# Performance work log

Measured on AMD Instinct MI355X. Metric: run time of the kernel, lower is better.

The kernel has to match this reference:

```python
import jax, jax.numpy as jnp
import numpy as np

NR_HEADS = 8


def segment_softmax(scores, indices, num_segments):
    # numerically stable softmax within each segment
    seg_max = jax.ops.segment_max(scores, indices, num_segments=num_segments)
    e = jnp.exp(scores - seg_max[indices])
    denom = jax.ops.segment_sum(e, indices, num_segments=num_segments)
    return e / denom[indices]


def setup_inputs() -> dict:
    key = jax.random.key(0)
    ks = jax.random.split(key, 10)
    n_ast, d, n_cfg = 500000, 128, 32768
    H, combined = NR_HEADS, 128
    w_scale = 1.0 / np.sqrt(d)
    return {
        "ast_nodes_encodings": jax.random.normal(ks[0], (n_ast, d), jnp.float32),
        "Wq": jax.random.normal(ks[1], (H, d, d), jnp.float32) * w_scale,
        "bq": jnp.zeros((H, d), jnp.float32),
        "Wk": jax.random.normal(ks[2], (H, d, d), jnp.float32) * w_scale,
        "bk": jnp.zeros((H, d), jnp.float32),
        "Wo": jax.random.normal(ks[3], (H * d, combined), jnp.float32) * (1.0 / np.sqrt(H * d)),
        "bo": jnp.zeros((combined,), jnp.float32),
        "ast_key": jax.random.randint(ks[4], (n_ast,), 0, n_ast, jnp.int32),
        "ast_value": jax.random.randint(ks[5], (n_ast,), 0, n_cfg, jnp.int32),
        "pdg_key": jnp.arange(n_cfg, dtype=jnp.int32),
        "pdg_value": jax.random.randint(ks[6], (n_cfg,), 0, n_ast, jnp.int32),
        "nr_cfg_nodes": n_cfg,
    }


def reference(ast_nodes_encodings, Wq, bq, Wk, bk, Wo, bo,
              ast_key, ast_value, pdg_key, pdg_value, nr_cfg_nodes):
    N = int(nr_cfg_nodes)
    d = ast_nodes_encodings.shape[1]
    inv_sqrt_d = 1.0 / np.sqrt(d)

    # Build per-PDG-node attention queries: gather sub-AST root encodings, scatter into [N, d]
    root_encodings = ast_nodes_encodings[pdg_value]                   # [N_map, d]
    attn_queries = jnp.zeros((N, d), ast_nodes_encodings.dtype).at[pdg_key].set(root_encodings)

    # Gather scattered inputs (one row per AST node assigned to a PDG node)
    values = ast_nodes_encodings[ast_key]                              # [E, d]
    indices = ast_value                                                # [E]

    # Multi-head scatter attention (ScatterCombiner with combining_method='attn')
    head_outs = []
    for h in range(NR_HEADS):  # small fixed head count; avoids [E, H, d] intermediates
        q = attn_queries @ Wq[h] + bq[h]                               # [N, d]
        k = values @ Wk[h] + bk[h]                                     # [E, d]
        scores = jnp.sum(q[indices] * k, axis=-1) * inv_sqrt_d         # [E]
        probs = segment_softmax(scores, indices, N)                    # [E]
        head_outs.append(jax.ops.segment_sum(probs[:, None] * values, indices, num_segments=N))

    combined = jnp.concatenate(head_outs, axis=-1) @ Wo + bo           # [N, combined_dim]
    return combined
```

## Files before the change

kernel.cpp:

```cpp
#include <hip/hip_runtime.h>
#include <hip/hip_bf16.h>
#include <cstdint>

typedef __hip_bfloat16 bf16;
typedef unsigned int uint;
typedef unsigned short ushort;

#define DEVI __device__ __forceinline__

DEVI float blo(uint u){ return __uint_as_float(u << 16); }
DEVI float bhi(uint u){ return __uint_as_float(u & 0xffff0000u); }
DEVI ushort f2b(float x){ uint u = __float_as_uint(x); uint r = (u + 0x7fffu + ((u >> 16) & 1u)) >> 16; return (ushort)r; }
DEVI uint pack2(float a, float b){ return (uint)f2b(a) | ((uint)f2b(b) << 16); }
DEVI float b2f(ushort h){ return __uint_as_float((uint)h << 16); }

typedef short bf16x8 __attribute__((ext_vector_type(8)));
typedef float f32x4  __attribute__((ext_vector_type(4)));

DEVI float grp8_sum(float x){
  int y;
  y = __builtin_amdgcn_update_dpp(0, __float_as_int(x), 0xB1, 0xF, 0xF, true);
  x += __int_as_float(y);
  y = __builtin_amdgcn_update_dpp(0, __float_as_int(x), 0x4E, 0xF, 0xF, true);
  x += __int_as_float(y);
  y = __builtin_amdgcn_update_dpp(0, __float_as_int(x), 0x141, 0xF, 0xF, true);
  x += __int_as_float(y);
  return x;
}

__global__ __launch_bounds__(256) void build_M(const float* __restrict__ Wq, const float* __restrict__ Wk,
                                               float* __restrict__ Mb){
  __shared__ float WkL[128*33];
  __shared__ float WqL[16*33];
  const int t = threadIdx.x;
  const int h = blockIdx.x >> 3, pg = blockIdx.x & 7, p0 = pg*16;
  const float* wk = Wk + (size_t)h*16384;
  const float* wq = Wq + ((size_t)h*128 + p0)*128;
  const int m = t & 127, half = t >> 7;
  float acc[8] = {0,0,0,0,0,0,0,0};
  for (int jc = 0; jc < 4; ++jc){
    __syncthreads();
    #pragma unroll
    for (int i = 0; i < 4; ++i){
      int g = t + 256*i;
      int mm = g >> 3, j0 = (g & 7)*4;
      float4 v = *(const float4*)(wk + mm*128 + jc*32 + j0);
      float* d = &WkL[mm*33 + j0];
      d[0] = v.x; d[1] = v.y; d[2] = v.z; d[3] = v.w;
    }
    {
      int e = t*2;
      int pr = e >> 5, jj = e & 31;
      float2 v = *(const float2*)(wq + pr*128 + jc*32 + jj);
      WqL[pr*33 + jj] = v.x; WqL[pr*33 + jj + 1] = v.y;
    }
    __syncthreads();
    for (int j = 0; j < 32; ++j){
      float wkv = WkL[m*33 + j];
      #pragma unroll
      for (int r = 0; r < 8; ++r)
        acc[r] = fmaf(WqL[(half*8 + r)*33 + j], wkv, acc[r]);
    }
  }
  #pragma unroll
  for (int r = 0; r < 8; ++r)
    Mb[(size_t)(p0 + half*8 + r)*1024 + h*128 + m] = acc[r];
}

__global__ void build_bias(const float* __restrict__ Wq, const float* __restrict__ Wk,
                           const float* __restrict__ bq, const float* __restrict__ bk,
                           float* __restrict__ cvec, float* __restrict__ uvec, float* __restrict__ sv){
  int h = blockIdx.x, m = threadIdx.x;
  const float* wkr = Wk + ((size_t)h*128 + m)*128;
  const float* wqr = Wq + ((size_t)h*128 + m)*128;
  const float* bqr = bq + h*128;
  const float* bkr = bk + h*128;
  float c = 0.f, u = 0.f;
  for (int j = 0; j < 128; ++j){
    c = fmaf(wkr[j], bqr[j], c);
    u = fmaf(wqr[j], bkr[j], u);
  }
  cvec[h*128 + m] = c;
  uvec[h*128 + m] = u;
  if (m == 0){
    float s = 0.f;
    for (int j = 0; j < 128; ++j) s = fmaf(bqr[j], bkr[j], s);
    sv[h] = s;
  }
}

__global__ void scatter_aq(const int* __restrict__ pk, const int* __restrict__ pv,
                           const float* __restrict__ ast, float* __restrict__ aq,
                           ushort* __restrict__ aqh, ushort* __restrict__ aql, int n_map){
  int i = blockIdx.x;
  if (i >= n_map) return;
  int k = pk[i], src = pv[i];
  int lane = threadIdx.x;
  float2 v = *(const float2*)(ast + (size_t)src*128 + 2*lane);
  *(float2*)(aq + (size_t)k*128 + 2*lane) = v;
  ushort h0 = f2b(v.x), h1 = f2b(v.y);
  ushort l0 = f2b(v.x - b2f(h0)), l1 = f2b(v.y - b2f(h1));
  *(uint*)(aqh + (size_t)k*128 + 2*lane) = (uint)h0 | ((uint)h1 << 16);
  *(uint*)(aql + (size_t)k*128 + 2*lane) = (uint)l0 | ((uint)l1 << 16);
}

__global__ void frag_pack(const float* __restrict__ S, uint4* __restrict__ D, int C, int ctn){
  const int b = blockIdx.x;
  const int ks = b / ctn, ct = b - ks*ctn;
  const int l = threadIdx.x;
  const int kb = ks*32 + (l >> 4)*8;
  const int c  = ct*16 + (l & 15);
  ushort hi[8], lo[8];
  #pragma unroll
  for (int j = 0; j < 8; ++j){
    float wv = S[(size_t)(kb + j)*C + c];
    ushort hh = f2b(wv);
    hi[j] = hh;
    lo[j] = f2b(wv - b2f(hh));
  }
  uint4 H, L;
  H.x = (uint)hi[0] | ((uint)hi[1] << 16);
  H.y = (uint)hi[2] | ((uint)hi[3] << 16);
  H.z = (uint)hi[4] | ((uint)hi[5] << 16);
  H.w = (uint)hi[6] | ((uint)hi[7] << 16);
  L.x = (uint)lo[0] | ((uint)lo[1] << 16);
  L.y = (uint)lo[2] | ((uint)lo[3] << 16);
  L.z = (uint)lo[4] | ((uint)lo[5] << 16);
  L.w = (uint)lo[6] | ((uint)lo[7] << 16);
  D[((size_t)b*2 + 0)*64 + l] = H;
  D[((size_t)b*2 + 1)*64 + l] = L;
}

__global__ __launch_bounds__(256, 1) void qt_mfma(const ushort* __restrict__ aqh, const ushort* __restrict__ aql,
                                                  const uint4* __restrict__ Mp, const float* __restrict__ cvec,
                                                  bf16* __restrict__ qt, int N){
  const int l = threadIdx.x & 63, w = threadIdx.x >> 6;
  const int lr = l & 15, lk = l >> 4;
  const int r0 = blockIdx.x*16;
  int ra = r0 + lr; if (ra > N-1) ra = N-1;
  const ushort* ph = aqh + (size_t)ra*128 + lk*8;
  const ushort* pl = aql + (size_t)ra*128 + lk*8;
  bf16x8 Ah[4], Al[4];
  #pragma unroll
  for (int ks = 0; ks < 4; ++ks){
    Ah[ks] = *(const bf16x8*)(ph + ks*32);
    Al[ks] = *(const bf16x8*)(pl + ks*32);
  }
  const int ct0 = w*16;
  for (int ct = 0; ct < 16; ++ct){
    const int ctg = ct0 + ct;
    f32x4 acc = {0.f, 0.f, 0.f, 0.f};
    #pragma unroll
    for (int ks = 0; ks < 4; ++ks){
      const uint4* q = Mp + ((size_t)(ks*64 + ctg)*2)*64 + l;
      bf16x8 Bh = *(const bf16x8*)q;
      bf16x8 Bl = *(const bf16x8*)(q + 64);
      acc = __builtin_amdgcn_mfma_f32_16x16x32_bf16(Ah[ks], Bh, acc, 0, 0, 0);
      acc = __builtin_amdgcn_mfma_f32_16x16x32_bf16(Al[ks], Bh, acc, 0, 0, 0);
      acc = __builtin_amdgcn_mfma_f32_16x16x32_bf16(Ah[ks], Bl, acc, 0, 0, 0);
    }
    const int cc = ctg*16 + lr;
    const float bv = cvec[cc];
    #pragma unroll
    for (int i = 0; i < 4; ++i){
      int rr = r0 + lk*4 + i;
      if (rr < N) ((ushort*)qt)[(size_t)rr*1024 + cc] = f2b(acc[i] + bv);
    }
  }
}

__global__ void qb_kernel(const float* __restrict__ aq, const float* __restrict__ uvec,
                          const float* __restrict__ sv, float* __restrict__ qb){
  int n = blockIdx.x, lane = threadIdx.x;
  int h = lane >> 3, g = lane & 7;
  const float* ar = aq + (size_t)n*128 + g*16;
  const float* ur = uvec + h*128 + g*16;
  float dot = 0.f;
  #pragma unroll
  for (int k = 0; k < 16; ++k) dot = fmaf(ar[k], ur[k], dot);
  dot += __shfl_xor(dot, 1);
  dot += __shfl_xor(dot, 2);
  dot += __shfl_xor(dot, 4);
  if (g == 0) qb[(size_t)n*8 + h] = dot + sv[h];
}

__global__ void count_edges(const int* __restrict__ av, int* __restrict__ counts, int E){
  int e = blockIdx.x*256 + threadIdx.x;
  if (e < E) atomicAdd(&counts[av[e]], 1);
}

__global__ void scan_offsets(const int* __restrict__ counts, int* __restrict__ offsets, int N){
  __shared__ int pa[1024];
  __shared__ int pb[1024];
  int t = threadIdx.x;
  int CH = (N + 1023) >> 10;
  int b = t*CH, e = b + CH;
  if (b > N) b = N;
  if (e > N) e = N;
  int s = 0;
  for (int i = b; i < e; ++i) s += counts[i];
  pa[t] = s;
  __syncthreads();
  int* src = pa; int* dst = pb;
  for (int off = 1; off < 1024; off <<= 1){
    int v = src[t];
    if (t >= off) v += src[t - off];
    __syncthreads();
    dst[t] = v;
    __syncthreads();
    int* tmp = src; src = dst; dst = tmp;
  }
  int run = src[t] - s;
  for (int i = b; i < e; ++i){ offsets[i] = run; run += counts[i]; }
  if (t == 1023) offsets[N] = src[1023];
}

__global__ void fill_edges(const int* __restrict__ av, const int* __restrict__ akey,
                           const int* __restrict__ offsets, int* __restrict__ cursor,
                           int* __restrict__ ridx, int E){
  int e = blockIdx.x*256 + threadIdx.x;
  if (e < E){
    int seg = av[e];
    int pos = offsets[seg] + atomicAdd(&cursor[seg], 1);
    ridx[pos] = akey[e];
  }
}

__global__ __launch_bounds__(256) void seg_attn(
    const bf16* __restrict__ qt, const float* __restrict__ qb,
    const int* __restrict__ offsets, const int* __restrict__ ridx,
    const float* __restrict__ ast, bf16* __restrict__ ho, int N)
{
  const int wid  = threadIdx.x >> 6;
  const int lane = threadIdx.x & 63;
  const int n = blockIdx.x*4 + wid;
  if (n >= N) return;
  const int beg = __builtin_amdgcn_readfirstlane(offsets[n]);
  const int end = __builtin_amdgcn_readfirstlane(offsets[n+1]);
  const int deg = end - beg;
  const int h = lane >> 3, g = lane & 7;

  const uint4* qp = (const uint4*)(qt + (size_t)n*1024 + h*128 + g*16);
  const uint4 qa = qp[0], qc = qp[1];
  const float4 q0 = make_float4(blo(qa.x), bhi(qa.x), blo(qa.y), bhi(qa.y));
  const float4 q1 = make_float4(blo(qa.z), bhi(qa.z), blo(qa.w), bhi(qa.w));
  const float4 q2 = make_float4(blo(qc.x), bhi(qc.x), blo(qc.y), bhi(qc.y));
  const float4 q3 = make_float4(blo(qc.z), bhi(qc.z), blo(qc.w), bhi(qc.w));
  const float qbv = qb[(size_t)n*8 + h];
  const float isd = 0.08838834764831845f;

  const int* rp = ridx + beg;

  float den = 0.f;
  float4 x0 = make_float4(0,0,0,0), x1 = x0, x2 = x0, x3 = x0;

  if (deg > 0){
    #define ROWP(ee) ((const float4*)(ast + (size_t)rp[(ee) < deg ? (ee) : deg-1]*128) + g*4)
    float4 A0, A1, A2, A3, B0, B1, B2, B3;
    { const float4* p = ROWP(0); A0 = p[0]; A1 = p[1]; A2 = p[2]; A3 = p[3]; }
    { const float4* p = ROWP(1); B0 = p[0]; B1 = p[1]; B2 = p[2]; B3 = p[3]; }
    int e = 0;
    for (; e + 1 < deg; e += 2){
      const float4 a0 = A0, a1 = A1, a2 = A2, a3 = A3;
      const float4 b0 = B0, b1 = B1, b2 = B2, b3 = B3;
      { const float4* p = ROWP(e + 2); A0 = p[0]; A1 = p[1]; A2 = p[2]; A3 = p[3]; }
      { const float4* p = ROWP(e + 3); B0 = p[0]; B1 = p[1]; B2 = p[2]; B3 = p[3]; }

      float dA = 0.f, dB = 0.f;
      dA = fmaf(a0.x, q0.x, dA); dA = fmaf(a0.y, q0.y, dA);
      dA = fmaf(a0.z, q0.z, dA); dA = fmaf(a0.w, q0.w, dA);
      dA = fmaf(a1.x, q1.x, dA); dA = fmaf(a1.y, q1.y, dA);
      dA = fmaf(a1.z, q1.z, dA); dA = fmaf(a1.w, q1.w, dA);
      dA = fmaf(a2.x, q2.x, dA); dA = fmaf(a2.y, q2.y, dA);
      dA = fmaf(a2.z, q2.z, dA); dA = fmaf(a2.w, q2.w, dA);
      dA = fmaf(a3.x, q3.x, dA); dA = fmaf(a3.y, q3.y, dA);
      dA = fmaf(a3.z, q3.z, dA); dA = fmaf(a3.w, q3.w, dA);
      dB = fmaf(b0.x, q0.x, dB); dB = fmaf(b0.y, q0.y, dB);
      dB = fmaf(b0.z, q0.z, dB); dB = fmaf(b0.w, q0.w, dB);
      dB = fmaf(b1.x, q1.x, dB); dB = fmaf(b1.y, q1.y, dB);
      dB = fmaf(b1.z, q1.z, dB); dB = fmaf(b1.w, q1.w, dB);
      dB = fmaf(b2.x, q2.x, dB); dB = fmaf(b2.y, q2.y, dB);
      dB = fmaf(b2.z, q2.z, dB); dB = fmaf(b2.w, q2.w, dB);
      dB = fmaf(b3.x, q3.x, dB); dB = fmaf(b3.y, q3.y, dB);
      dB = fmaf(b3.z, q3.z, dB); dB = fmaf(b3.w, q3.w, dB);
      dA = grp8_sum(dA);
      dB = grp8_sum(dB);

      const float pA = __expf((dA + qbv) * isd);
      const float pB = __expf((dB + qbv) * isd);
      den += pA; den += pB;

      x0.x = fmaf(pA, a0.x, x0.x); x0.y = fmaf(pA, a0.y, x0.y);
      x0.z = fmaf(pA, a0.z, x0.z); x0.w = fmaf(pA, a0.w, x0.w);
      x1.x = fmaf(pA, a1.x, x1.x); x1.y = fmaf(pA, a1.y, x1.y);
      x1.z = fmaf(pA, a1.z, x1.z); x1.w = fmaf(pA, a1.w, x1.w);
      x2.x = fmaf(pA, a2.x, x2.x); x2.y = fmaf(pA, a2.y, x2.y);
      x2.z = fmaf(pA, a2.z, x2.z); x2.w = fmaf(pA, a2.w, x2.w);
      x3.x = fmaf(pA, a3.x, x3.x); x3.y = fmaf(pA, a3.y, x3.y);
      x3.z = fmaf(pA, a3.z, x3.z); x3.w = fmaf(pA, a3.w, x3.w);
      x0.x = fmaf(pB, b0.x, x0.x); x0.y = fmaf(pB, b0.y, x0.y);
      x0.z = fmaf(pB, b0.z, x0.z); x0.w = fmaf(pB, b0.w, x0.w);
      x1.x = fmaf(pB, b1.x, x1.x); x1.y = fmaf(pB, b1.y, x1.y);
      x1.z = fmaf(pB, b1.z, x1.z); x1.w = fmaf(pB, b1.w, x1.w);
      x2.x = fmaf(pB, b2.x, x2.x); x2.y = fmaf(pB, b2.y, x2.y);
      x2.z = fmaf(pB, b2.z, x2.z); x2.w = fmaf(pB, b2.w, x2.w);
      x3.x = fmaf(pB, b3.x, x3.x); x3.y = fmaf(pB, b3.y, x3.y);
      x3.z = fmaf(pB, b3.z, x3.z); x3.w = fmaf(pB, b3.w, x3.w);
    }
    if (e < deg){
      const float4 a0 = A0, a1 = A1, a2 = A2, a3 = A3;
      float dA = 0.f;
      dA = fmaf(a0.x, q0.x, dA); dA = fmaf(a0.y, q0.y, dA);
      dA = fmaf(a0.z, q0.z, dA); dA = fmaf(a0.w, q0.w, dA);
      dA = fmaf(a1.x, q1.x, dA); dA = fmaf(a1.y, q1.y, dA);
      dA = fmaf(a1.z, q1.z, dA); dA = fmaf(a1.w, q1.w, dA);
      dA = fmaf(a2.x, q2.x, dA); dA = fmaf(a2.y, q2.y, dA);
      dA = fmaf(a2.z, q2.z, dA); dA = fmaf(a2.w, q2.w, dA);
      dA = fmaf(a3.x, q3.x, dA); dA = fmaf(a3.y, q3.y, dA);
      dA = fmaf(a3.z, q3.z, dA); dA = fmaf(a3.w, q3.w, dA);
      dA = grp8_sum(dA);
      const float pA = __expf((dA + qbv) * isd);
      den += pA;
      x0.x = fmaf(pA, a0.x, x0.x); x0.y = fmaf(pA, a0.y, x0.y);
      x0.z = fmaf(pA, a0.z, x0.z); x0.w = fmaf(pA, a0.w, x0.w);
      x1.x = fmaf(pA, a1.x, x1.x); x1.y = fmaf(pA, a1.y, x1.y);
      x1.z = fmaf(pA, a1.z, x1.z); x1.w = fmaf(pA, a1.w, x1.w);
      x2.x = fmaf(pA, a2.x, x2.x); x2.y = fmaf(pA, a2.y, x2.y);
      x2.z = fmaf(pA, a2.z, x2.z); x2.w = fmaf(pA, a2.w, x2.w);
      x3.x = fmaf(pA, a3.x, x3.x); x3.y = fmaf(pA, a3.y, x3.y);
      x3.z = fmaf(pA, a3.z, x3.z); x3.w = fmaf(pA, a3.w, x3.w);
    }
    #undef ROWP
  }
  const float r = (deg > 0) ? (1.f / den) : 0.f;

  uint4 o0, o1;
  o0.x = pack2(x0.x*r, x0.y*r); o0.y = pack2(x0.z*r, x0.w*r);
  o0.z = pack2(x1.x*r, x1.y*r); o0.w = pack2(x1.z*r, x1.w*r);
  o1.x = pack2(x2.x*r, x2.y*r); o1.y = pack2(x2.z*r, x2.w*r);
  o1.z = pack2(x3.x*r, x3.y*r); o1.w = pack2(x3.z*r, x3.w*r);
  uint4* hb = (uint4*)(ho + (size_t)n*1024 + h*128 + g*16);
  hb[0] = o0;
  hb[1] = o1;
}

__global__ __launch_bounds__(256, 1) void out_mfma(const bf16* __restrict__ ho, const uint4* __restrict__ Wp,
                                                   const float* __restrict__ bo, float* __restrict__ out, int N){
  const int l = threadIdx.x & 63, w = threadIdx.x >> 6;
  const int lr = l & 15, lk = l >> 4;
  const int r0 = blockIdx.x*128 + w*32;
  int ra = r0 + lr;      if (ra > N-1) ra = N-1;
  int rb = r0 + 16 + lr; if (rb > N-1) rb = N-1;
  const bf16* pa = ho + (size_t)ra*1024 + lk*8;
  const bf16* pb = ho + (size_t)rb*1024 + lk*8;
  const uint4* pw = Wp + l;

  f32x4 acc[2][8];
  #pragma unroll
  for (int i = 0; i < 2; ++i)
    #pragma unroll
    for (int c = 0; c < 8; ++c)
      #pragma unroll
      for (int j = 0; j < 4; ++j) acc[i][c][j] = 0.f;

  bf16x8 Aa[2], Ab[2], Ba[16], Bb[16];

  auto LD = [&](int ks, bf16x8* A, bf16x8* B){
    A[0] = *(const bf16x8*)(pa + ks*32);
    A[1] = *(const bf16x8*)(pb + ks*32);
    const uint4* q = pw + (size_t)ks*1024;
    #pragma unroll
    for (int u = 0; u < 16; ++u) B[u] = *(const bf16x8*)(q + (size_t)u*64);
  };
  auto MM = [&](bf16x8* A, bf16x8* B){
    #pragma unroll
    for (int c = 0; c < 8; ++c){
      acc[0][c] = __builtin_amdgcn_mfma_f32_16x16x32_bf16(A[0], B[2*c],   acc[0][c], 0, 0, 0);
      acc[1][c] = __builtin_amdgcn_mfma_f32_16x16x32_bf16(A[1], B[2*c],   acc[1][c], 0, 0, 0);
      acc[0][c] = __builtin_amdgcn_mfma_f32_16x16x32_bf16(A[0], B[2*c+1], acc[0][c], 0, 0, 0);
      acc[1][c] = __builtin_amdgcn_mfma_f32_16x16x32_bf16(A[1], B[2*c+1], acc[1][c], 0, 0, 0);
    }
  };

  LD(0, Aa, Ba);
  for (int ks = 0; ks < 32; ks += 2){
    LD(ks + 1, Ab, Bb);
    MM(Aa, Ba);
    if (ks + 2 < 32) LD(ks + 2, Aa, Ba);
    MM(Ab, Bb);
  }

  #pragma unroll
  for (int c = 0; c < 8; ++c){
    float bv = bo[c*16 + lr];
    #pragma unroll
    for (int rt = 0; rt < 2; ++rt){
      #pragma unroll
      for (int i = 0; i < 4; ++i){
        int rr = r0 + rt*16 + lk*4 + i;
        if (rr < N) out[(size_t)rr*128 + c*16 + lr] = acc[rt][c][i] + bv;
      }
    }
  }
}

extern "C" void kernel_launch(void* const* d_in, const int* in_sizes, int n_in,
                              void* d_out, int out_size, void* d_ws, size_t ws_size,
                              hipStream_t stream) {
  const float* ast = (const float*)d_in[0];
  const float* Wq  = (const float*)d_in[1];
  const float* bq  = (const float*)d_in[2];
  const float* Wk  = (const float*)d_in[3];
  const float* bk  = (const float*)d_in[4];
  const float* Wo  = (const float*)d_in[5];
  const float* bo  = (const float*)d_in[6];
  const int* ast_key   = (const int*)d_in[7];
  const int* ast_value = (const int*)d_in[8];
  const int* pdg_key   = (const int*)d_in[9];
  const int* pdg_value = (const int*)d_in[10];
  const int E     = in_sizes[7];
  const int n_map = in_sizes[9];
  const int N     = out_size / 128;
  float* out = (float*)d_out;

  char* w = (char*)d_ws;
  auto carve = [&](size_t bytes)->char*{
    char* p = w; w += (bytes + 255) & ~size_t(255); return p;
  };
  bf16*  qt      = (bf16*) carve((size_t)N*1024*2);
  float* aq      = (float*)carve((size_t)N*128*4);
  float* Mb      = (float*)carve((size_t)128*1024*4);
  float* cvec    = (float*)carve(1024*4);
  float* uvec    = (float*)carve(1024*4);
  float* sv      = (float*)carve(8*4);
  float* qb      = (float*)carve((size_t)N*8*4);
  int*   counts  = (int*)  carve((size_t)N*4);
  int*   offsets = (int*)  carve((size_t)(N+1)*4);
  int*   cursor  = (int*)  carve((size_t)N*4);
  int*   ridx    = (int*)  carve((size_t)E*4);
  bf16*  ho      = (bf16*) carve((size_t)N*1024*2);
  uint4* Wp      = (uint4*)carve((size_t)256*2*64*16);
  ushort* aqh    = (ushort*)carve((size_t)N*128*2);
  ushort* aql    = (ushort*)carve((size_t)N*128*2);
  uint4* Mp      = (uint4*)carve((size_t)256*2*64*16);
  (void)ws_size; (void)n_in;

  hipMemsetAsync(aq,     0, (size_t)N*128*4, stream);
  hipMemsetAsync(aqh,    0, (size_t)N*128*2, stream);
  hipMemsetAsync(aql,    0, (size_t)N*128*2, stream);
  hipMemsetAsync(counts, 0, (size_t)N*4, stream);
  hipMemsetAsync(cursor, 0, (size_t)N*4, stream);

  build_M   <<<64, 256, 0, stream>>>(Wq, Wk, Mb);
  build_bias<<<8, 128, 0, stream>>>(Wq, Wk, bq, bk, cvec, uvec, sv);
  frag_pack <<<256, 64, 0, stream>>>(Wo, Wp, 128, 8);
  scatter_aq<<<n_map, 64, 0, stream>>>(pdg_key, pdg_value, ast, aq, aqh, aql, n_map);
  frag_pack <<<256, 64, 0, stream>>>(Mb, Mp, 1024, 64);
  qt_mfma   <<<(N + 15)/16, 256, 0, stream>>>(aqh, aql, Mp, cvec, qt, N);
  qb_kernel <<<N, 64, 0, stream>>>(aq, uvec, sv, qb);
  count_edges<<<(E + 255)/256, 256, 0, stream>>>(ast_value, counts, E);
  scan_offsets<<<1, 1024, 0, stream>>>(counts, offsets, N);
  fill_edges<<<(E + 255)/256, 256, 0, stream>>>(ast_value, ast_key, offsets, cursor, ridx, E);
  seg_attn  <<<(N + 3)/4, 256, 0, stream>>>(qt, qb, offsets, ridx, ast, ho, N);
  out_mfma  <<<(N + 127)/128, 256, 0, stream>>>(ho, Wp, bo, out, N);
}
```

Measured before the change: 770.8 us.

## Retile qt_mfma for B reuse and remap seg_attn lanes to two heads

qt_mfma now gives each wave 32 rows and all 64 column tiles, double-buffering the packed M fragments so each B load feeds two row tiles instead of one. seg_attn maps 16 lanes per pair of heads, so each lane reads 8 floats of an AST row once and uses them for two heads. The per-head dot product is reduced across 16 lanes with row-shift DPP, exp is folded into exp2 with a prescaled constant, and up to six rows are prefetched ahead. The aim is less redundant global traffic for the M fragments and the gathered AST rows, and more loads in flight, at the cost of higher register pressure.

```diff
diff --git a/kernel.cpp b/kernel.cpp
--- a/kernel.cpp
+++ b/kernel.cpp
@@ -17,14 +17,12 @@
 typedef short bf16x8 __attribute__((ext_vector_type(8)));
 typedef float f32x4  __attribute__((ext_vector_type(4)));
 
-DEVI float grp8_sum(float x){
+DEVI float row16_sum(float x){
   int y;
-  y = __builtin_amdgcn_update_dpp(0, __float_as_int(x), 0xB1, 0xF, 0xF, true);
-  x += __int_as_float(y);
-  y = __builtin_amdgcn_update_dpp(0, __float_as_int(x), 0x4E, 0xF, 0xF, true);
-  x += __int_as_float(y);
-  y = __builtin_amdgcn_update_dpp(0, __float_as_int(x), 0x141, 0xF, 0xF, true);
-  x += __int_as_float(y);
+  y = __builtin_amdgcn_update_dpp(0, __float_as_int(x), 0x121, 0xF, 0xF, true); x += __int_as_float(y);
+  y = __builtin_amdgcn_update_dpp(0, __float_as_int(x), 0x122, 0xF, 0xF, true); x += __int_as_float(y);
+  y = __builtin_amdgcn_update_dpp(0, __float_as_int(x), 0x124, 0xF, 0xF, true); x += __int_as_float(y);
+  y = __builtin_amdgcn_update_dpp(0, __float_as_int(x), 0x128, 0xF, 0xF, true); x += __int_as_float(y);
   return x;
 }
 
@@ -136,36 +134,57 @@
                                                   bf16* __restrict__ qt, int N){
   const int l = threadIdx.x & 63, w = threadIdx.x >> 6;
   const int lr = l & 15, lk = l >> 4;
-  const int r0 = blockIdx.x*16;
-  int ra = r0 + lr; if (ra > N-1) ra = N-1;
-  const ushort* ph = aqh + (size_t)ra*128 + lk*8;
-  const ushort* pl = aql + (size_t)ra*128 + lk*8;
-  bf16x8 Ah[4], Al[4];
+  const int r0 = blockIdx.x*128 + w*32;
+  int ra = r0 + lr;      if (ra > N-1) ra = N-1;
+  int rb = r0 + 16 + lr; if (rb > N-1) rb = N-1;
+
+  bf16x8 Ah0[4], Al0[4], Ah1[4], Al1[4];
   #pragma unroll
   for (int ks = 0; ks < 4; ++ks){
-    Ah[ks] = *(const bf16x8*)(ph + ks*32);
-    Al[ks] = *(const bf16x8*)(pl + ks*32);
-  }
-  const int ct0 = w*16;
-  for (int ct = 0; ct < 16; ++ct){
-    const int ctg = ct0 + ct;
-    f32x4 acc = {0.f, 0.f, 0.f, 0.f};
+    Ah0[ks] = *(const bf16x8*)(aqh + (size_t)ra*128 + lk*8 + ks*32);
+    Al0[ks] = *(const bf16x8*)(aql + (size_t)ra*128 + lk*8 + ks*32);
+    Ah1[ks] = *(const bf16x8*)(aqh + (size_t)rb*128 + lk*8 + ks*32);
+    Al1[ks] = *(const bf16x8*)(aql + (size_t)rb*128 + lk*8 + ks*32);
+  }
+  const uint4* pw = Mp + l;
+
+  bf16x8 Ba[8], Bb[8];
+  auto LDB = [&](int ct, bf16x8* B){
     #pragma unroll
     for (int ks = 0; ks < 4; ++ks){
-      const uint4* q = Mp + ((size_t)(ks*64 + ctg)*2)*64 + l;
-      bf16x8 Bh = *(const bf16x8*)q;
-      bf16x8 Bl = *(const bf16x8*)(q + 64);
-      acc = __builtin_amdgcn_mfma_f32_16x16x32_bf16(Ah[ks], Bh, acc, 0, 0, 0);
-      acc = __builtin_amdgcn_mfma_f32_16x16x32_bf16(Al[ks], Bh, acc, 0, 0, 0);
-      acc = __builtin_amdgcn_mfma_f32_16x16x32_bf16(Ah[ks], Bl, acc, 0, 0, 0);
-    }
-    const int cc = ctg*16 + lr;
+      const uint4* q = pw + ((size_t)(ks*64 + ct)*2)*64;
+      B[ks*2]   = *(const bf16x8*)q;
+      B[ks*2+1] = *(const bf16x8*)(q + 64);
+    }
+  };
+  auto DO = [&](int ct, bf16x8* B){
+    f32x4 a0 = {0.f,0.f,0.f,0.f}, a1 = {0.f,0.f,0.f,0.f};
+    #pragma unroll
+    for (int ks = 0; ks < 4; ++ks){
+      a0 = __builtin_amdgcn_mfma_f32_16x16x32_bf16(Ah0[ks], B[2*ks],   a0, 0, 0, 0);
+      a1 = __builtin_amdgcn_mfma_f32_16x16x32_bf16(Ah1[ks], B[2*ks],   a1, 0, 0, 0);
+      a0 = __builtin_amdgcn_mfma_f32_16x16x32_bf16(Al0[ks], B[2*ks],   a0, 0, 0, 0);
+      a1 = __builtin_amdgcn_mfma_f32_16x16x32_bf16(Al1[ks], B[2*ks],   a1, 0, 0, 0);
+      a0 = __builtin_amdgcn_mfma_f32_16x16x32_bf16(Ah0[ks], B[2*ks+1], a0, 0, 0, 0);
+      a1 = __builtin_amdgcn_mfma_f32_16x16x32_bf16(Ah1[ks], B[2*ks+1], a1, 0, 0, 0);
+    }
+    const int cc = ct*16 + lr;
     const float bv = cvec[cc];
     #pragma unroll
     for (int i = 0; i < 4; ++i){
-      int rr = r0 + lk*4 + i;
-      if (rr < N) ((ushort*)qt)[(size_t)rr*1024 + cc] = f2b(acc[i] + bv);
-    }
+      int rr0 = r0 + lk*4 + i;
+      if (rr0 < N) ((ushort*)qt)[(size_t)rr0*1024 + cc] = f2b(a0[i] + bv);
+      int rr1 = r0 + 16 + lk*4 + i;
+      if (rr1 < N) ((ushort*)qt)[(size_t)rr1*1024 + cc] = f2b(a1[i] + bv);
+    }
+  };
+
+  LDB(0, Ba);
+  for (int ct = 0; ct < 64; ct += 2){
+    LDB(ct + 1, Bb);
+    DO(ct, Ba);
+    if (ct + 2 < 64) LDB(ct + 2, Ba);
+    DO(ct + 1, Bb);
   }
 }
 
@@ -238,110 +257,86 @@
   const int beg = __builtin_amdgcn_readfirstlane(offsets[n]);
   const int end = __builtin_amdgcn_readfirstlane(offsets[n+1]);
   const int deg = end - beg;
-  const int h = lane >> 3, g = lane & 7;
-
-  const uint4* qp = (const uint4*)(qt + (size_t)n*1024 + h*128 + g*16);
-  const uint4 qa = qp[0], qc = qp[1];
-  const float4 q0 = make_float4(blo(qa.x), bhi(qa.x), blo(qa.y), bhi(qa.y));
-  const float4 q1 = make_float4(blo(qa.z), bhi(qa.z), blo(qa.w), bhi(qa.w));
-  const float4 q2 = make_float4(blo(qc.x), bhi(qc.x), blo(qc.y), bhi(qc.y));
-  const float4 q3 = make_float4(blo(qc.z), bhi(qc.z), blo(qc.w), bhi(qc.w));
-  const float qbv = qb[(size_t)n*8 + h];
-  const float isd = 0.08838834764831845f;
+  const int grp = lane >> 4, d4 = lane & 15;
+  const int h0 = 2*grp, h1 = 2*grp + 1;
+
+  const ushort* qtp = (const ushort*)qt + (size_t)n*1024 + d4*8;
+  const uint4 Qa = *(const uint4*)(qtp + h0*128);
+  const uint4 Qb = *(const uint4*)(qtp + h1*128);
+  const float4 q0lo = make_float4(blo(Qa.x), bhi(Qa.x), blo(Qa.y), bhi(Qa.y));
+  const float4 q0hi = make_float4(blo(Qa.z), bhi(Qa.z), blo(Qa.w), bhi(Qa.w));
+  const float4 q1lo = make_float4(blo(Qb.x), bhi(Qb.x), blo(Qb.y), bhi(Qb.y));
+  const float4 q1hi = make_float4(blo(Qb.z), bhi(Qb.z), blo(Qb.w), bhi(Qb.w));
+  const float SC = 0.12751744886681336f;
+  const float qs0 = qb[(size_t)n*8 + h0] * SC;
+  const float qs1 = qb[(size_t)n*8 + h1] * SC;
 
   const int* rp = ridx + beg;
 
-  float den = 0.f;
-  float4 x0 = make_float4(0,0,0,0), x1 = x0, x2 = x0, x3 = x0;
+  float den0 = 0.f, den1 = 0.f;
+  float4 x0lo = make_float4(0,0,0,0), x0hi = x0lo, x1lo = x0lo, x1hi = x0lo;
 
   if (deg > 0){
-    #define ROWP(ee) ((const float4*)(ast + (size_t)rp[(ee) < deg ? (ee) : deg-1]*128) + g*4)
-    float4 A0, A1, A2, A3, B0, B1, B2, B3;
-    { const float4* p = ROWP(0); A0 = p[0]; A1 = p[1]; A2 = p[2]; A3 = p[3]; }
-    { const float4* p = ROWP(1); B0 = p[0]; B1 = p[1]; B2 = p[2]; B3 = p[3]; }
+#define LOADP(Pa0, Pa1, Pb0, Pb1, base) do { \
+    int iA = (base) < deg ? (base) : deg-1; \
+    int iB = (base)+1 < deg ? (base)+1 : deg-1; \
+    const float4* pA = (const float4*)(ast + (size_t)rp[iA]*128 + d4*8); \
+    const float4* pB = (const float4*)(ast + (size_t)rp[iB]*128 + d4*8); \
+    Pa0 = pA[0]; Pa1 = pA[1]; Pb0 = pB[0]; Pb1 = pB[1]; } while(0)
+
+#define C1(A0, A1) do { \
+    float s0, s1; \
+    s0 = A0.x*q0lo.x; s0 = fmaf(A0.y, q0lo.y, s0); s0 = fmaf(A0.z, q0lo.z, s0); s0 = fmaf(A0.w, q0lo.w, s0); \
+    s0 = fmaf(A1.x, q0hi.x, s0); s0 = fmaf(A1.y, q0hi.y, s0); s0 = fmaf(A1.z, q0hi.z, s0); s0 = fmaf(A1.w, q0hi.w, s0); \
+    s1 = A0.x*q1lo.x; s1 = fmaf(A0.y, q1lo.y, s1); s1 = fmaf(A0.z, q1lo.z, s1); s1 = fmaf(A0.w, q1lo.w, s1); \
+    s1 = fmaf(A1.x, q1hi.x, s1); s1 = fmaf(A1.y, q1hi.y, s1); s1 = fmaf(A1.z, q1hi.z, s1); s1 = fmaf(A1.w, q1hi.w, s1); \
+    s0 = row16_sum(s0); s1 = row16_sum(s1); \
+    const float p0 = exp2f(fmaf(s0, SC, qs0)); \
+    const float p1 = exp2f(fmaf(s1, SC, qs1)); \
+    den0 += p0; den1 += p1; \
+    x0lo.x = fmaf(p0, A0.x, x0lo.x); x0lo.y = fmaf(p0, A0.y, x0lo.y); \
+    x0lo.z = fmaf(p0, A0.z, x0lo.z); x0lo.w = fmaf(p0, A0.w, x0lo.w); \
+    x0hi.x = fmaf(p0, A1.x, x0hi.x); x0hi.y = fmaf(p0, A1.y, x0hi.y); \
+    x0hi.z = fmaf(p0, A1.z, x0hi.z); x0hi.w = fmaf(p0, A1.w, x0hi.w); \
+    x1lo.x = fmaf(p1, A0.x, x1lo.x); x1lo.y = fmaf(p1, A0.y, x1lo.y); \
+    x1lo.z = fmaf(p1, A0.z, x1lo.z); x1lo.w = fmaf(p1, A0.w, x1lo.w); \
+    x1hi.x = fmaf(p1, A1.x, x1hi.x); x1hi.y = fmaf(p1, A1.y, x1hi.y); \
+    x1hi.z = fmaf(p1, A1.z, x1hi.z); x1hi.w = fmaf(p1, A1.w, x1hi.w); \
+  } while(0)
+
+    float4 P0a0, P0a1, P0b0, P0b1;
+    float4 P1a0, P1a1, P1b0, P1b1;
+    float4 P2a0, P2a1, P2b0, P2b1;
+    LOADP(P0a0, P0a1, P0b0, P0b1, 0);
+    LOADP(P1a0, P1a1, P1b0, P1b1, 2);
+    LOADP(P2a0, P2a1, P2b0, P2b1, 4);
     int e = 0;
-    for (; e + 1 < deg; e += 2){
-      const float4 a0 = A0, a1 = A1, a2 = A2, a3 = A3;
-      const float4 b0 = B0, b1 = B1, b2 = B2, b3 = B3;
-      { const float4* p = ROWP(e + 2); A0 = p[0]; A1 = p[1]; A2 = p[2]; A3 = p[3]; }
-      { const float4* p = ROWP(e + 3); B0 = p[0]; B1 = p[1]; B2 = p[2]; B3 = p[3]; }
-
-      float dA = 0.f, dB = 0.f;
-      dA = fmaf(a0.x, q0.x, dA); dA = fmaf(a0.y, q0.y, dA);
-      dA = fmaf(a0.z, q0.z, dA); dA = fmaf(a0.w, q0.w, dA);
-      dA = fmaf(a1.x, q1.x, dA); dA = fmaf(a1.y, q1.y, dA);
-      dA = fmaf(a1.z, q1.z, dA); dA = fmaf(a1.w, q1.w, dA);
-      dA = fmaf(a2.x, q2.x, dA); dA = fmaf(a2.y, q2.y, dA);
-      dA = fmaf(a2.z, q2.z, dA); dA = fmaf(a2.w, q2.w, dA);
-      dA = fmaf(a3.x, q3.x, dA); dA = fmaf(a3.y, q3.y, dA);
-      dA = fmaf(a3.z, q3.z, dA); dA = fmaf(a3.w, q3.w, dA);
-      dB = fmaf(b0.x, q0.x, dB); dB = fmaf(b0.y, q0.y, dB);
-      dB = fmaf(b0.z, q0.z, dB); dB = fmaf(b0.w, q0.w, dB);
-      dB = fmaf(b1.x, q1.x, dB); dB = fmaf(b1.y, q1.y, dB);
-      dB = fmaf(b1.z, q1.z, dB); dB = fmaf(b1.w, q1.w, dB);
-      dB = fmaf(b2.x, q2.x, dB); dB = fmaf(b2.y, q2.y, dB);
-      dB = fmaf(b2.z, q2.z, dB); dB = fmaf(b2.w, q2.w, dB);
-      dB = fmaf(b3.x, q3.x, dB); dB = fmaf(b3.y, q3.y, dB);
-      dB = fmaf(b3.z, q3.z, dB); dB = fmaf(b3.w, q3.w, dB);
-      dA = grp8_sum(dA);
-      dB = grp8_sum(dB);
-
-      const float pA = __expf((dA + qbv) * isd);
-      const float pB = __expf((dB + qbv) * isd);
-      den += pA; den += pB;
-
-      x0.x = fmaf(pA, a0.x, x0.x); x0.y = fmaf(pA, a0.y, x0.y);
-      x0.z = fmaf(pA, a0.z, x0.z); x0.w = fmaf(pA, a0.w, x0.w);
-      x1.x = fmaf(pA, a1.x, x1.x); x1.y = fmaf(pA, a1.y, x1.y);
-      x1.z = fmaf(pA, a1.z, x1.z); x1.w = fmaf(pA, a1.w, x1.w);
-      x2.x = fmaf(pA, a2.x, x2.x); x2.y = fmaf(pA, a2.y, x2.y);
-      x2.z = fmaf(pA, a2.z, x2.z); x2.w = fmaf(pA, a2.w, x2.w);
-      x3.x = fmaf(pA, a3.x, x3.x); x3.y = fmaf(pA, a3.y, x3.y);
-      x3.z = fmaf(pA, a3.z, x3.z); x3.w = fmaf(pA, a3.w, x3.w);
-      x0.x = fmaf(pB, b0.x, x0.x); x0.y = fmaf(pB, b0.y, x0.y);
-      x0.z = fmaf(pB, b0.z, x0.z); x0.w = fmaf(pB, b0.w, x0.w);
-      x1.x = fmaf(pB, b1.x, x1.x); x1.y = fmaf(pB, b1.y, x1.y);
-      x1.z = fmaf(pB, b1.z, x1.z); x1.w = fmaf(pB, b1.w, x1.w);
-      x2.x = fmaf(pB, b2.x, x2.x); x2.y = fmaf(pB, b2.y, x2.y);
-      x2.z = fmaf(pB, b2.z, x2.z); x2.w = fmaf(pB, b2.w, x2.w);
-      x3.x = fmaf(pB, b3.x, x3.x); x3.y = fmaf(pB, b3.y, x3.y);
-      x3.z = fmaf(pB, b3.z, x3.z); x3.w = fmaf(pB, b3.w, x3.w);
-    }
-    if (e < deg){
-      const float4 a0 = A0, a1 = A1, a2 = A2, a3 = A3;
-      float dA = 0.f;
-      dA = fmaf(a0.x, q0.x, dA); dA = fmaf(a0.y, q0.y, dA);
-      dA = fmaf(a0.z, q0.z, dA); dA = fmaf(a0.w, q0.w, dA);
-      dA = fmaf(a1.x, q1.x, dA); dA = fmaf(a1.y, q1.y, dA);
-      dA = fmaf(a1.z, q1.z, dA); dA = fmaf(a1.w, q1.w, dA);
-      dA = fmaf(a2.x, q2.x, dA); dA = fmaf(a2.y, q2.y, dA);
-      dA = fmaf(a2.z, q2.z, dA); dA = fmaf(a2.w, q2.w, dA);
-      dA = fmaf(a3.x, q3.x, dA); dA = fmaf(a3.y, q3.y, dA);
-      dA = fmaf(a3.z, q3.z, dA); dA = fmaf(a3.w, q3.w, dA);
-      dA = grp8_sum(dA);
-      const float pA = __expf((dA + qbv) * isd);
-      den += pA;
-      x0.x = fmaf(pA, a0.x, x0.x); x0.y = fmaf(pA, a0.y, x0.y);
-      x0.z = fmaf(pA, a0.z, x0.z); x0.w = fmaf(pA, a0.w, x0.w);
-      x1.x = fmaf(pA, a1.x, x1.x); x1.y = fmaf(pA, a1.y, x1.y);
-      x1.z = fmaf(pA, a1.z, x1.z); x1.w = fmaf(pA, a1.w, x1.w);
-      x2.x = fmaf(pA, a2.x, x2.x); x2.y = fmaf(pA, a2.y, x2.y);
-      x2.z = fmaf(pA, a2.z, x2.z); x2.w = fmaf(pA, a2.w, x2.w);
-      x3.x = fmaf(pA, a3.x, x3.x); x3.y = fmaf(pA, a3.y, x3.y);
-      x3.z = fmaf(pA, a3.z, x3.z); x3.w = fmaf(pA, a3.w, x3.w);
-    }
-    #undef ROWP
-  }
-  const float r = (deg > 0) ? (1.f / den) : 0.f;
+    for (; e + 5 < deg; e += 6){
+      C1(P0a0, P0a1); C1(P0b0, P0b1); LOADP(P0a0, P0a1, P0b0, P0b1, e + 6);
+      C1(P1a0, P1a1); C1(P1b0, P1b1); LOADP(P1a0, P1a1, P1b0, P1b1, e + 8);
+      C1(P2a0, P2a1); C1(P2b0, P2b1); LOADP(P2a0, P2a1, P2b0, P2b1, e + 10);
+    }
+    const int t = deg - e;
+    if (t >= 1) C1(P0a0, P0a1);
+    if (t >= 2) C1(P0b0, P0b1);
+    if (t >= 3) C1(P1a0, P1a1);
+    if (t >= 4) C1(P1b0, P1b1);
+    if (t >= 5) C1(P2a0, P2a1);
+    if (t >= 6) C1(P2b0, P2b1);
+#undef C1
+#undef LOADP
+  }
+  const float r0v = (deg > 0) ? (1.f / den0) : 0.f;
+  const float r1v = (deg > 0) ? (1.f / den1) : 0.f;
 
   uint4 o0, o1;
-  o0.x = pack2(x0.x*r, x0.y*r); o0.y = pack2(x0.z*r, x0.w*r);
-  o0.z = pack2(x1.x*r, x1.y*r); o0.w = pack2(x1.z*r, x1.w*r);
-  o1.x = pack2(x2.x*r, x2.y*r); o1.y = pack2(x2.z*r, x2.w*r);
-  o1.z = pack2(x3.x*r, x3.y*r); o1.w = pack2(x3.z*r, x3.w*r);
-  uint4* hb = (uint4*)(ho + (size_t)n*1024 + h*128 + g*16);
-  hb[0] = o0;
-  hb[1] = o1;
+  o0.x = pack2(x0lo.x*r0v, x0lo.y*r0v); o0.y = pack2(x0lo.z*r0v, x0lo.w*r0v);
+  o0.z = pack2(x0hi.x*r0v, x0hi.y*r0v); o0.w = pack2(x0hi.z*r0v, x0hi.w*r0v);
+  o1.x = pack2(x1lo.x*r1v, x1lo.y*r1v); o1.y = pack2(x1lo.z*r1v, x1lo.w*r1v);
+  o1.z = pack2(x1hi.x*r1v, x1hi.y*r1v); o1.w = pack2(x1hi.z*r1v, x1hi.w*r1v);
+  ushort* hb = (ushort*)ho + (size_t)n*1024 + d4*8;
+  *(uint4*)(hb + h0*128) = o0;
+  *(uint4*)(hb + h1*128) = o1;
 }
 
 __global__ __launch_bounds__(256, 1) void out_mfma(const bf16* __restrict__ ho, const uint4* __restrict__ Wp,
@@ -456,7 +451,7 @@
   frag_pack <<<256, 64, 0, stream>>>(Wo, Wp, 128, 8);
   scatter_aq<<<n_map, 64, 0, stream>>>(pdg_key, pdg_value, ast, aq, aqh, aql, n_map);
   frag_pack <<<256, 64, 0, stream>>>(Mb, Mp, 1024, 64);
-  qt_mfma   <<<(N + 15)/16, 256, 0, stream>>>(aqh, aql, Mp, cvec, qt, N);
+  qt_mfma   <<<(N + 127)/128, 256, 0, stream>>>(aqh, aql, Mp, cvec, qt, N);
   qb_kernel <<<N, 64, 0, stream>>>(aq, uvec, sv, qb);
   count_edges<<<(E + 255)/256, 256, 0, stream>>>(ast_value, counts, E);
   scan_offsets<<<1, 1024, 0, stream>>>(counts, offsets, N);
```

Result: no change. 756.7 us (-1.8%).
